# Kernel tuning notes

Hardware: AMD Instinct MI355X
Metric: run time of the kernel (lower is better)

## Reference

```python
import jax, jax.numpy as jnp
import numpy as np

DIM, HEADS, K = 128, 4, 7
HD = DIM // HEADS


def _nbr_idx(n, k):
    # NATTEN boundary-clamped neighborhood (dilation=1): window start clamped to [0, n-k]
    i = np.arange(n)
    start = np.clip(i - k // 2, 0, n - k)
    idx = start[:, None] + np.arange(k)[None, :]          # (n, k) absolute neighbor index
    rel = idx - i[:, None] + (k - 1)                      # (n, k) index into 2k-1 rpb axis
    return jnp.asarray(idx), jnp.asarray(rel)


def _ln(x, w, b, eps=1e-5):
    mu = jnp.mean(x, -1, keepdims=True)
    var = jnp.var(x, -1, keepdims=True)
    return (x - mu) * jax.lax.rsqrt(var + eps) * w + b


def setup_inputs() -> dict:
    key = jax.random.key(0)
    ks = jax.random.split(key, 16)
    B, H, W, C = 1, 128, 128, DIM
    f = jax.random.normal
    inp = {
        'x': f(ks[0], (B, H, W, C), jnp.float32),
        'y': f(ks[1], (B, H, W, C), jnp.float32),
        'qv_w': f(ks[2], (2 * C, C), jnp.float32) * 0.02,
        'qv_b': jnp.zeros((2 * C,), jnp.float32),
        'k_w': f(ks[3], (C, C), jnp.float32) * 0.02,
        'k_b': jnp.zeros((C,), jnp.float32),
        'rpb': f(ks[4], (HEADS, 2 * K - 1, 2 * K - 1), jnp.float32) * 0.02,
        'proj_w': f(ks[5], (C, C), jnp.float32) * 0.02,
        'proj_b': jnp.zeros((C,), jnp.float32),
        'n1_w': jnp.ones((C,), jnp.float32),
        'n1_b': jnp.zeros((C,), jnp.float32),
        'n2_w': jnp.ones((C,), jnp.float32),
        'n2_b': jnp.zeros((C,), jnp.float32),
        'fc1_w': f(ks[6], (4 * C, C), jnp.float32) * 0.02,
        'fc1_b': jnp.zeros((4 * C,), jnp.float32),
        'fc2_w': f(ks[7], (C, 4 * C), jnp.float32) * 0.02,
        'fc2_b': jnp.zeros((C,), jnp.float32),
    }
    return inp


def _block(x, y, qv_w, qv_b, k_w, k_b, rpb, proj_w, proj_b,
           n1_w, n1_b, n2_w, n2_b, fc1_w, fc1_b, fc2_w, fc2_b):
    B, H, W, C = x.shape
    scale = HD ** -0.5
    # ---- CrossNat2D attention on norm1(x) vs y ----
    xn = _ln(x, n1_w, n1_b)
    qv = xn @ qv_w.T + qv_b                               # (B,H,W,2C)
    q = qv[..., :C].reshape(B, H, W, HEADS, HD) * scale
    v = qv[..., C:].reshape(B, H, W, HEADS, HD)
    k = (y @ k_w.T + k_b).reshape(B, H, W, HEADS, HD)

    idx_h, rel_h = _nbr_idx(H, K)
    idx_w, rel_w = _nbr_idx(W, K)
    # gather neighborhoods: (B, H, K, W, K, HEADS, HD)
    k_nbr = k[:, idx_h][:, :, :, idx_w]
    v_nbr = v[:, idx_h][:, :, :, idx_w]

    # attention logits over KxK neighborhood
    attn = jnp.einsum('bijhd,biajchd->bijhac', q, k_nbr)  # (B,H,W,heads,K,K)
    bias = rpb[:, rel_h][..., rel_w]                      # (heads,H,K,W,K)
    attn = attn + jnp.transpose(bias, (1, 3, 0, 2, 4))    # broadcast over B
    attn = jax.nn.softmax(attn.reshape(B, H, W, HEADS, K * K), axis=-1)
    attn = attn.reshape(B, H, W, HEADS, K, K)

    out = jnp.einsum('bijhac,biajchd->bijhd', attn, v_nbr).reshape(B, H, W, C)
    out = out @ proj_w.T + proj_b

    x = x + out
    # ---- MLP ----
    h = _ln(x, n2_w, n2_b) @ fc1_w.T + fc1_b
    h = jax.nn.gelu(h, approximate=False) @ fc2_w.T + fc2_b
    return x + h


def reference(x, y, qv_w, qv_b, k_w, k_b, rpb, proj_w, proj_b,
              n1_w, n1_b, n2_w, n2_b, fc1_w, fc1_b, fc2_w, fc2_b):
    return _block(x, y, qv_w, qv_b, k_w, k_b, rpb, proj_w, proj_b,
                  n1_w, n1_b, n2_w, n2_b, fc1_w, fc1_b, fc2_w, fc2_b)
```

## Files before the change

kernel.cpp:

```cpp
#include <hip/hip_runtime.h>
#include <hip/hip_bf16.h>


#define N_PIX 16384
#define C 128
#define HEADS 4
#define HD 32
#define HW 128

typedef __hip_bfloat16 bf16;
typedef __attribute__((ext_vector_type(8))) short bf16x8;
typedef __attribute__((ext_vector_type(4))) float f32x4;

__device__ __forceinline__ short f2bs(float f) {
    unsigned int r;
    asm("v_cvt_pk_bf16_f32 %0, %1, %2" : "=v"(r) : "v"(f), "v"(f));
    return (short)(r & 0xffff);
}
__device__ __forceinline__ unsigned int pack2(float a, float b) {
    unsigned int r;
    asm("v_cvt_pk_bf16_f32 %0, %1, %2" : "=v"(r) : "v"(a), "v"(b));
    return r;
}
__device__ __forceinline__ float bs2f(short s) {
    __hip_bfloat16_raw r; r.x = (unsigned short)s;
    return __bfloat162float(__hip_bfloat16(r));
}
__device__ __forceinline__ float gelu_f(float v) {
    const float z2 = v * (2.302236206f + 0.102943322f * v * v);
    return v / (1.f + exp2f(-z2));
}

__global__ __launch_bounds__(256) void k_wconv(
    const float* __restrict__ qv_w, const float* __restrict__ k_w,
    const float* __restrict__ proj_w, const float* __restrict__ fc1_w,
    const float* __restrict__ fc2_w,
    short* __restrict__ wqv, short* __restrict__ wk, short* __restrict__ wproj,
    short* __restrict__ wfc1, short* __restrict__ wfc2) {
    const int i = blockIdx.x * 256 + threadIdx.x;
    if (i < 32768) wqv[i] = f2bs(qv_w[i]);
    if (i < 16384) { wk[i] = f2bs(k_w[i]); wproj[i] = f2bs(proj_w[i]); }
    if (i < 65536) { wfc1[i] = f2bs(fc1_w[i]); wfc2[i] = f2bs(fc2_w[i]); }
}

__global__ __launch_bounds__(256, 4) void k_qkv(
    const float* __restrict__ x, const float* __restrict__ y,
    const short* __restrict__ wqv, const float* __restrict__ qv_b,
    const short* __restrict__ wk, const float* __restrict__ k_b,
    const float* __restrict__ n1_w, const float* __restrict__ n1_b,
    bf16* __restrict__ qb, bf16* __restrict__ vb, bf16* __restrict__ kb) {
    __shared__ short xn[16][136];
    __shared__ short yl[16][136];
    const int t = threadIdx.x;
    const int pix0 = (blockIdx.x & 7) * 2048 + (blockIdx.x >> 3) * 16;
    {
        const int r = t >> 4, ch8 = (t & 15) * 8;
        const size_t gp = (size_t)(pix0 + r) * C + ch8;
        float xv[8], yv[8];
        *(float4*)&xv[0] = *(const float4*)(x + gp);
        *(float4*)&xv[4] = *(const float4*)(x + gp + 4);
        *(float4*)&yv[0] = *(const float4*)(y + gp);
        *(float4*)&yv[4] = *(const float4*)(y + gp + 4);
        float sm = 0.f, sq = 0.f;
#pragma unroll
        for (int i2 = 0; i2 < 8; i2++) { sm += xv[i2]; sq += xv[i2] * xv[i2]; }
#pragma unroll
        for (int msk = 1; msk < 16; msk <<= 1) {
            sm += __shfl_xor(sm, msk, 64); sq += __shfl_xor(sq, msk, 64);
        }
        const float mu = sm * (1.f / 128.f);
        const float ri = rsqrtf(sq * (1.f / 128.f) - mu * mu + 1e-5f);
        float w1[8], b1[8];
        *(float4*)&w1[0] = *(const float4*)(n1_w + ch8);
        *(float4*)&w1[4] = *(const float4*)(n1_w + ch8 + 4);
        *(float4*)&b1[0] = *(const float4*)(n1_b + ch8);
        *(float4*)&b1[4] = *(const float4*)(n1_b + ch8 + 4);
        uint4 xp, yp;
        xp.x = pack2((xv[0] - mu) * ri * w1[0] + b1[0], (xv[1] - mu) * ri * w1[1] + b1[1]);
        xp.y = pack2((xv[2] - mu) * ri * w1[2] + b1[2], (xv[3] - mu) * ri * w1[3] + b1[3]);
        xp.z = pack2((xv[4] - mu) * ri * w1[4] + b1[4], (xv[5] - mu) * ri * w1[5] + b1[5]);
        xp.w = pack2((xv[6] - mu) * ri * w1[6] + b1[6], (xv[7] - mu) * ri * w1[7] + b1[7]);
        yp.x = pack2(yv[0], yv[1]); yp.y = pack2(yv[2], yv[3]);
        yp.z = pack2(yv[4], yv[5]); yp.w = pack2(yv[6], yv[7]);
        *(uint4*)&xn[r][ch8] = xp;
        *(uint4*)&yl[r][ch8] = yp;
    }
    __syncthreads();
    const int wave = t >> 6, lane = t & 63, quad = lane >> 4, l15 = lane & 15;
    const float scale = 0.1767766952966369f;
    {
        bf16x8 aA[4];
#pragma unroll
        for (int kt = 0; kt < 4; kt++)
            aA[kt] = *(const bf16x8*)&xn[l15][kt * 32 + quad * 8];
#pragma unroll
        for (int s = 0; s < 4; s++) {
            const int n = (wave + 4 * s) * 16 + l15;
            f32x4 acc = {0.f, 0.f, 0.f, 0.f};
#pragma unroll
            for (int kt = 0; kt < 4; kt++) {
                bf16x8 b = *(const bf16x8*)&wqv[n * C + kt * 32 + quad * 8];
                acc = __builtin_amdgcn_mfma_f32_16x16x32_bf16(aA[kt], b, acc, 0, 0, 0);
            }
            const float bias = qv_b[n];
#pragma unroll
            for (int r = 0; r < 4; r++) {
                const int m = quad * 4 + r;
                const float v = acc[r] + bias;
                if (s < 2) qb[(size_t)(pix0 + m) * C + n] = __float2bfloat16(v * scale);
                else       vb[(size_t)(pix0 + m) * C + (n - C)] = __float2bfloat16(v);
            }
        }
    }
    {
        bf16x8 aY[4];
#pragma unroll
        for (int kt = 0; kt < 4; kt++)
            aY[kt] = *(const bf16x8*)&yl[l15][kt * 32 + quad * 8];
        const int n0 = (wave * 2) * 16 + l15, n1 = (wave * 2 + 1) * 16 + l15;
        f32x4 a0 = {0.f, 0.f, 0.f, 0.f}, a1 = {0.f, 0.f, 0.f, 0.f};
#pragma unroll
        for (int kt = 0; kt < 4; kt++) {
            bf16x8 b0 = *(const bf16x8*)&wk[n0 * C + kt * 32 + quad * 8];
            bf16x8 b1 = *(const bf16x8*)&wk[n1 * C + kt * 32 + quad * 8];
            a0 = __builtin_amdgcn_mfma_f32_16x16x32_bf16(aY[kt], b0, a0, 0, 0, 0);
            a1 = __builtin_amdgcn_mfma_f32_16x16x32_bf16(aY[kt], b1, a1, 0, 0, 0);
        }
        const float b0s = k_b[n0], b1s = k_b[n1];
#pragma unroll
        for (int r = 0; r < 4; r++) {
            const int m = quad * 4 + r;
            kb[(size_t)(pix0 + m) * C + n0] = __float2bfloat16(a0[r] + b0s);
            kb[(size_t)(pix0 + m) * C + n1] = __float2bfloat16(a1[r] + b1s);
        }
    }
}

__global__ __launch_bounds__(512, 4) void k_fam(
    const bf16* __restrict__ qb, const bf16* __restrict__ kb,
    const bf16* __restrict__ vb, const float* __restrict__ rpb,
    const float* __restrict__ x,
    const short* __restrict__ wproj, const float* __restrict__ proj_b,
    const float* __restrict__ n2_w, const float* __restrict__ n2_b,
    const short* __restrict__ wfc1, const float* __restrict__ fc1_b,
    const short* __restrict__ wfc2, const float* __restrict__ fc2_b,
    float* __restrict__ out) {
    __shared__ short KP[19008];
    __shared__ short Vl[19008];
    __shared__ float muA[32], riA[32];
    short* const Pm  = KP;
    short* const aoL = KP;
    short* const x1b = KP + 4352;
    short* const xnb = KP + 8704;
    short* const hb  = Vl;
    const int t = threadIdx.x;
    const int wave = t >> 6, lane = t & 63, quad = lane >> 4, l15 = lane & 15;
    const int h = wave & 3, mt = wave >> 2;
    const int s_ = blockIdx.x >> 3;
    const int i0 = ((blockIdx.x & 7) * 2 + (s_ >> 5)) * 8;
    const int j0 = (s_ & 31) * 4;
    const int rs = min(max(i0 - 3, 0), 114);
    const int cs = min(max(j0 - 3, 0), 118);
    const int mA = mt * 16 + l15;
    const int pA = (i0 + (mA >> 2)) * HW + j0 + (mA & 3);
    const bf16x8 aQ = *(const bf16x8*)(qb + (size_t)pA * C + h * HD + quad * 8);
    const int nR0 = h * 16 + l15, nR1 = (h + 4) * 16 + l15;
    float xres0[4], xres1[4];
#pragma unroll
    for (int r = 0; r < 4; r++) {
        const int m = mt * 16 + quad * 4 + r;
        const int p = (i0 + (m >> 2)) * HW + j0 + (m & 3);
        xres0[r] = x[(size_t)p * C + nR0];
        xres1[r] = x[(size_t)p * C + nR1];
    }
    {
        const int seg = t & 15, r0 = t >> 4;
        const int q0 = (r0 * 13) >> 7;
        const int m0 = r0 - q0 * 10;
#pragma unroll
        for (int half = 0; half < 2; half++) {
            const bf16* __restrict__ src = half ? vb : kb;
            short* const dst = half ? Vl : KP;
            int r = r0, q = q0, rm = m0;
#pragma unroll
            for (int it = 0; it < 5; it++) {
                if (r < 140) {
                    const size_t g = (size_t)((rs + q) * HW + cs + rm) * C + seg * 8;
                    *(uint4*)&dst[r * 132 + seg * 8] = *(const uint4*)(src + g);
                }
                r += 32; q += 3; rm += 2;
                if (rm >= 10) { rm -= 10; q += 1; }
            }
        }
    }
    __syncthreads();
    f32x4 S[9];
#pragma unroll
    for (int nt = 0; nt < 9; nt++) {
        const bf16x8 bK = *(const bf16x8*)&KP[(nt * 16 + l15) * 132 + h * HD + quad * 8];
        f32x4 z = {0.f, 0.f, 0.f, 0.f};
        S[nt] = __builtin_amdgcn_mfma_f32_16x16x32_bf16(aQ, bK, z, 0, 0, 0);
    }
    const float* rpbh = rpb + h * 169;
    int aiA[9], ajA[9];
    {
        int ai = rs + (l15 >= 10 ? 1 : 0);
        int aj = cs + (l15 >= 10 ? l15 - 10 : l15);
        const int cb = cs + 10;
#pragma unroll
        for (int nt = 0; nt < 9; nt++) {
            aiA[nt] = ai; ajA[nt] = aj;
            aj += 6; ai += 1;
            if (aj >= cb) { aj -= 10; ai += 1; }
        }
    }
    float smx[4];
#pragma unroll
    for (int r = 0; r < 4; r++) {
        const int m = mt * 16 + quad * 4 + r;
        const int i = i0 + (m >> 2), j = j0 + (m & 3);
        const int shi = min(max(i - 3, 0), 121);
        const int swj = min(max(j - 3, 0), 121);
        float best = -1e30f;
#pragma unroll
        for (int nt = 0; nt < 9; nt++) {
            const int ai = aiA[nt], aj = ajA[nt];
            const bool vnb = (nt < 8) | (l15 < 12);
            const bool valid = vnb & (ai >= shi) & (ai <= shi + 6) & (aj >= swj) & (aj <= swj + 6);
            const int ri = min(max(ai - i + 6, 0), 12);
            const int rj = min(max(aj - j + 6, 0), 12);
            const float v = valid ? (S[nt][r] + rpbh[ri * 13 + rj]) : -1e30f;
            S[nt][r] = v;
            best = fmaxf(best, v);
        }
        for (int msk = 1; msk < 16; msk <<= 1) best = fmaxf(best, __shfl_xor(best, msk, 64));
        float s = 0.f;
#pragma unroll
        for (int nt = 0; nt < 9; nt++) {
            const float e = __expf(S[nt][r] - best);
            S[nt][r] = e;
            s += e;
        }
        for (int msk = 1; msk < 16; msk <<= 1) s += __shfl_xor(s, msk, 64);
        smx[r] = 1.f / s;
    }
    __syncthreads();
#pragma unroll
    for (int r = 0; r < 4; r++) {
        short* prow = &Pm[(wave * 16 + quad * 4 + r) * 144];
#pragma unroll
        for (int nt = 0; nt < 9; nt++)
            prow[nt * 16 + l15] = f2bs(S[nt][r] * smx[r]);
    }
    f32x4 O0 = {0.f, 0.f, 0.f, 0.f}, O1 = {0.f, 0.f, 0.f, 0.f};
#pragma unroll
    for (int kt = 0; kt < 4; kt++) {
        const bf16x8 aP = *(const bf16x8*)&Pm[(wave * 16 + l15) * 144 + kt * 32 + quad * 8];
#pragma unroll
        for (int nt2 = 0; nt2 < 2; nt2++) {
            const int ch = h * HD + nt2 * 16 + l15;
            const int base = (kt * 32 + quad * 8) * 132 + ch;
            bf16x8 bV;
#pragma unroll
            for (int jj = 0; jj < 8; jj++) bV[jj] = Vl[base + jj * 132];
            if (nt2 == 0) O0 = __builtin_amdgcn_mfma_f32_16x16x32_bf16(aP, bV, O0, 0, 0, 0);
            else          O1 = __builtin_amdgcn_mfma_f32_16x16x32_bf16(aP, bV, O1, 0, 0, 0);
        }
    }
    {
        const bf16x8 aP = *(const bf16x8*)&Pm[(wave * 16 + l15) * 144 + 128 + quad * 8];
#pragma unroll
        for (int nt2 = 0; nt2 < 2; nt2++) {
            const int ch = h * HD + nt2 * 16 + l15;
            bf16x8 bV = {0, 0, 0, 0, 0, 0, 0, 0};
            if (quad == 0) {
                const int base = 128 * 132 + ch;
#pragma unroll
                for (int jj = 0; jj < 8; jj++) bV[jj] = Vl[base + jj * 132];
            } else if (quad == 1) {
                const int base = 136 * 132 + ch;
#pragma unroll
                for (int jj = 0; jj < 4; jj++) bV[jj] = Vl[base + jj * 132];
            }
            if (nt2 == 0) O0 = __builtin_amdgcn_mfma_f32_16x16x32_bf16(aP, bV, O0, 0, 0, 0);
            else          O1 = __builtin_amdgcn_mfma_f32_16x16x32_bf16(aP, bV, O1, 0, 0, 0);
        }
    }
    bf16x8 wp0[4], wp1[4];
#pragma unroll
    for (int kt = 0; kt < 4; kt++) {
        wp0[kt] = *(const bf16x8*)&wproj[nR0 * C + kt * 32 + quad * 8];
        wp1[kt] = *(const bf16x8*)&wproj[nR1 * C + kt * 32 + quad * 8];
    }
    __syncthreads();
#pragma unroll
    for (int r = 0; r < 4; r++) {
        const int m = mt * 16 + quad * 4 + r;
        aoL[m * 136 + h * HD + l15] = f2bs(O0[r]);
        aoL[m * 136 + h * HD + 16 + l15] = f2bs(O1[r]);
    }
    __syncthreads();
    float x1f0[4], x1f1[4];
    {
        bf16x8 aO[4];
#pragma unroll
        for (int kt = 0; kt < 4; kt++)
            aO[kt] = *(const bf16x8*)&aoL[(mt * 16 + l15) * 136 + kt * 32 + quad * 8];
        f32x4 a0 = {0.f, 0.f, 0.f, 0.f}, a1 = {0.f, 0.f, 0.f, 0.f};
#pragma unroll
        for (int kt = 0; kt < 4; kt++) {
            a0 = __builtin_amdgcn_mfma_f32_16x16x32_bf16(aO[kt], wp0[kt], a0, 0, 0, 0);
            a1 = __builtin_amdgcn_mfma_f32_16x16x32_bf16(aO[kt], wp1[kt], a1, 0, 0, 0);
        }
        const float b0s = proj_b[nR0], b1s = proj_b[nR1];
#pragma unroll
        for (int r = 0; r < 4; r++) {
            const int m = mt * 16 + quad * 4 + r;
            const float v0 = xres0[r] + a0[r] + b0s;
            const float v1 = xres1[r] + a1[r] + b1s;
            x1f0[r] = v0; x1f1[r] = v1;
            x1b[m * 136 + nR0] = f2bs(v0);
            x1b[m * 136 + nR1] = f2bs(v1);
        }
    }
    __syncthreads();
    {
        const int r = t >> 4, c8 = (t & 15) * 8;
        const short* p = &x1b[r * 136 + c8];
        float sm = 0.f, sq = 0.f;
#pragma unroll
        for (int i2 = 0; i2 < 8; i2++) {
            const float v = bs2f(p[i2]); sm += v; sq += v * v;
        }
#pragma unroll
        for (int msk = 1; msk < 16; msk <<= 1) {
            sm += __shfl_xor(sm, msk, 64); sq += __shfl_xor(sq, msk, 64);
        }
        if ((t & 15) == 0) {
            const float mu = sm * (1.f / 128.f);
            const float var = sq * (1.f / 128.f) - mu * mu;
            muA[r] = mu; riA[r] = rsqrtf(var + 1e-5f);
        }
    }
    __syncthreads();
    for (int e = t; e < 32 * 128; e += 512) {
        const int r = e >> 7, c = e & 127;
        xnb[r * 136 + c] = f2bs((bs2f(x1b[r * 136 + c]) - muA[r]) * riA[r] * n2_w[c] + n2_b[c]);
    }
    __syncthreads();
    {
        bf16x8 aX[4];
#pragma unroll
        for (int kt = 0; kt < 4; kt++)
            aX[kt] = *(const bf16x8*)&xnb[(mt * 16 + l15) * 136 + kt * 32 + quad * 8];
#pragma unroll
        for (int a = 0; a < 4; a++) {
            const int n0 = (h + 8 * a) * 16 + l15, n1 = (h + 8 * a + 4) * 16 + l15;
            f32x4 a0 = {0.f, 0.f, 0.f, 0.f}, a1 = {0.f, 0.f, 0.f, 0.f};
#pragma unroll
            for (int kt = 0; kt < 4; kt++) {
                bf16x8 b0 = *(const bf16x8*)&wfc1[n0 * C + kt * 32 + quad * 8];
                bf16x8 b1 = *(const bf16x8*)&wfc1[n1 * C + kt * 32 + quad * 8];
                a0 = __builtin_amdgcn_mfma_f32_16x16x32_bf16(aX[kt], b0, a0, 0, 0, 0);
                a1 = __builtin_amdgcn_mfma_f32_16x16x32_bf16(aX[kt], b1, a1, 0, 0, 0);
            }
            const float b0s = fc1_b[n0], b1s = fc1_b[n1];
#pragma unroll
            for (int r = 0; r < 4; r++) {
                const int m = mt * 16 + quad * 4 + r;
                hb[m * 520 + n0] = f2bs(gelu_f(a0[r] + b0s));
                hb[m * 520 + n1] = f2bs(gelu_f(a1[r] + b1s));
            }
        }
    }
    __syncthreads();
    {
        f32x4 a0 = {0.f, 0.f, 0.f, 0.f}, a1 = {0.f, 0.f, 0.f, 0.f};
#pragma unroll
        for (int kt = 0; kt < 16; kt++) {
            const bf16x8 aP = *(const bf16x8*)&hb[(mt * 16 + l15) * 520 + kt * 32 + quad * 8];
            bf16x8 b0 = *(const bf16x8*)&wfc2[nR0 * 512 + kt * 32 + quad * 8];
            bf16x8 b1 = *(const bf16x8*)&wfc2[nR1 * 512 + kt * 32 + quad * 8];
            a0 = __builtin_amdgcn_mfma_f32_16x16x32_bf16(aP, b0, a0, 0, 0, 0);
            a1 = __builtin_amdgcn_mfma_f32_16x16x32_bf16(aP, b1, a1, 0, 0, 0);
        }
        const float b0s = fc2_b[nR0], b1s = fc2_b[nR1];
#pragma unroll
        for (int r = 0; r < 4; r++) {
            const int m = mt * 16 + quad * 4 + r;
            const int p = (i0 + (m >> 2)) * HW + j0 + (m & 3);
            out[(size_t)p * C + nR0] = a0[r] + b0s + x1f0[r];
            out[(size_t)p * C + nR1] = a1[r] + b1s + x1f1[r];
        }
    }
}

extern "C" void kernel_launch(void* const* d_in, const int* in_sizes, int n_in,
                              void* d_out, int out_size, void* d_ws, size_t ws_size,
                              hipStream_t stream) {
    const float* x      = (const float*)d_in[0];
    const float* y      = (const float*)d_in[1];
    const float* qv_w   = (const float*)d_in[2];
    const float* qv_b   = (const float*)d_in[3];
    const float* k_w    = (const float*)d_in[4];
    const float* k_b    = (const float*)d_in[5];
    const float* rpb    = (const float*)d_in[6];
    const float* proj_w = (const float*)d_in[7];
    const float* proj_b = (const float*)d_in[8];
    const float* n1_w   = (const float*)d_in[9];
    const float* n1_b   = (const float*)d_in[10];
    const float* n2_w   = (const float*)d_in[11];
    const float* n2_b   = (const float*)d_in[12];
    const float* fc1_w  = (const float*)d_in[13];
    const float* fc1_b  = (const float*)d_in[14];
    const float* fc2_w  = (const float*)d_in[15];
    const float* fc2_b  = (const float*)d_in[16];
    float* out = (float*)d_out;

    bf16* qb  = (bf16*)d_ws;
    bf16* vb  = qb + (size_t)N_PIX * C;
    bf16* kb  = vb + (size_t)N_PIX * C;
    short* wqv  = (short*)(kb + (size_t)N_PIX * C);
    short* wk   = wqv + 32768;
    short* wproj= wk + 16384;
    short* wfc1 = wproj + 16384;
    short* wfc2 = wfc1 + 65536;

    k_wconv<<<256, 256, 0, stream>>>(qv_w, k_w, proj_w, fc1_w, fc2_w,
                                     wqv, wk, wproj, wfc1, wfc2);
    k_qkv<<<1024, 256, 0, stream>>>(x, y, wqv, qv_b, wk, k_b, n1_w, n1_b,
                                    qb, vb, kb);
    k_fam<<<512, 512, 0, stream>>>(qb, kb, vb, rpb, x, wproj, proj_b, n2_w, n2_b,
                                   wfc1, fc1_b, wfc2, fc2_b, out);
}
```

Before: 160.4 us.

## Enlarge fused attention+MLP tile to 8x8 pixels with shared 14x14 K/V halo

```diff
diff --git a/kernel.cpp b/kernel.cpp
--- a/kernel.cpp
+++ b/kernel.cpp
@@ -136,7 +136,7 @@
     }
 }
 
-__global__ __launch_bounds__(512, 4) void k_fam(
+__global__ __launch_bounds__(512, 2) void k_fam(
     const bf16* __restrict__ qb, const bf16* __restrict__ kb,
     const bf16* __restrict__ vb, const float* __restrict__ rpb,
     const float* __restrict__ x,
@@ -145,252 +145,318 @@
     const short* __restrict__ wfc1, const float* __restrict__ fc1_b,
     const short* __restrict__ wfc2, const float* __restrict__ fc2_b,
     float* __restrict__ out) {
-    __shared__ short KP[19008];
-    __shared__ short Vl[19008];
-    __shared__ float muA[32], riA[32];
-    short* const Pm  = KP;
-    short* const aoL = KP;
-    short* const x1b = KP + 4352;
-    short* const xnb = KP + 8704;
-    short* const hb  = Vl;
+    __shared__ short SH[67104];
+    short* const KU  = SH;
+    short* const VU  = SH + 25872;
+    short* const Pb  = SH + 51744;
+    short* const aoL = SH;
+    short* const xnb = SH + 8448;
+    short* const hb  = SH + 16896;
+    short* const x1b = SH + 51744;
     const int t = threadIdx.x;
     const int wave = t >> 6, lane = t & 63, quad = lane >> 4, l15 = lane & 15;
     const int h = wave & 3, mt = wave >> 2;
-    const int s_ = blockIdx.x >> 3;
-    const int i0 = ((blockIdx.x & 7) * 2 + (s_ >> 5)) * 8;
-    const int j0 = (s_ & 31) * 4;
+    const int p = wave & 1, g = wave >> 1;
+    const int tile = (blockIdx.x & 7) * 32 + (blockIdx.x >> 3);
+    const int i0 = (tile >> 4) * 8, j0 = (tile & 15) * 8;
     const int rs = min(max(i0 - 3, 0), 114);
-    const int cs = min(max(j0 - 3, 0), 118);
-    const int mA = mt * 16 + l15;
-    const int pA = (i0 + (mA >> 2)) * HW + j0 + (mA & 3);
-    const bf16x8 aQ = *(const bf16x8*)(qb + (size_t)pA * C + h * HD + quad * 8);
-    const int nR0 = h * 16 + l15, nR1 = (h + 4) * 16 + l15;
-    float xres0[4], xres1[4];
-#pragma unroll
-    for (int r = 0; r < 4; r++) {
-        const int m = mt * 16 + quad * 4 + r;
-        const int p = (i0 + (m >> 2)) * HW + j0 + (m & 3);
-        xres0[r] = x[(size_t)p * C + nR0];
-        xres1[r] = x[(size_t)p * C + nR1];
+    const int cs2 = min(max(j0 - 3, 0), 114);
+    const int n_0 = (2 * g) * 16 + l15, n_1 = (2 * g + 1) * 16 + l15;
+    bf16x8 aQv[2];
+#pragma unroll
+    for (int u = 0; u < 2; u++) {
+        const int q = mt * 2 + u;
+        const int iq = i0 + (q >> 1) * 4, jq = j0 + (q & 1) * 4;
+        const int pA = (iq + (l15 >> 2)) * HW + jq + (l15 & 3);
+        aQv[u] = *(const bf16x8*)(qb + (size_t)pA * C + h * HD + quad * 8);
+    }
+    float xres[2][2][4];
+#pragma unroll
+    for (int u = 0; u < 2; u++) {
+        const int qm = 2 * p + u;
+        const int ib = i0 + (qm >> 1) * 4 + quad, jb = j0 + (qm & 1) * 4;
+#pragma unroll
+        for (int r = 0; r < 4; r++) {
+            const size_t pp = (size_t)(ib * HW + jb + r) * C;
+            xres[u][0][r] = x[pp + n_0];
+            xres[u][1][r] = x[pp + n_1];
+        }
     }
     {
         const int seg = t & 15, r0 = t >> 4;
-        const int q0 = (r0 * 13) >> 7;
-        const int m0 = r0 - q0 * 10;
-#pragma unroll
-        for (int half = 0; half < 2; half++) {
-            const bf16* __restrict__ src = half ? vb : kb;
-            short* const dst = half ? Vl : KP;
-            int r = r0, q = q0, rm = m0;
-#pragma unroll
-            for (int it = 0; it < 5; it++) {
-                if (r < 140) {
-                    const size_t g = (size_t)((rs + q) * HW + cs + rm) * C + seg * 8;
-                    *(uint4*)&dst[r * 132 + seg * 8] = *(const uint4*)(src + g);
+        int q14 = (r0 >= 28) ? 2 : (r0 >= 14 ? 1 : 0);
+        int m14 = r0 - 14 * q14;
+        int r = r0;
+#pragma unroll
+        for (int it = 0; it < 7; it++) {
+            if (r < 196) {
+                const size_t gp = (size_t)((rs + q14) * HW + (cs2 + m14)) * C + seg * 8;
+                *(uint4*)&KU[r * 132 + seg * 8] = *(const uint4*)(kb + gp);
+                *(uint4*)&VU[r * 132 + seg * 8] = *(const uint4*)(vb + gp);
+            }
+            r += 32; q14 += 2; m14 += 4;
+            if (m14 >= 14) { m14 -= 14; q14 += 1; }
+        }
+    }
+    int nrA[7], ncA[7];
+    {
+        int nr = (l15 >= 10) ? 1 : 0;
+        int nc = l15 - ((l15 >= 10) ? 10 : 0);
+#pragma unroll
+        for (int nt = 0; nt < 7; nt++) {
+            nrA[nt] = nr; ncA[nt] = nc;
+            nc += 6; nr += 1;
+            if (nc >= 10) { nc -= 10; nr += 1; }
+        }
+    }
+    __syncthreads();
+    const float* rpbh = rpb + h * 169;
+    f32x4 Oacc[2][2];
+#pragma unroll
+    for (int u = 0; u < 2; u++) {
+        Oacc[u][0] = (f32x4){0.f, 0.f, 0.f, 0.f};
+        Oacc[u][1] = (f32x4){0.f, 0.f, 0.f, 0.f};
+    }
+#pragma unroll
+    for (int u = 0; u < 2; u++) {
+        const int q = mt * 2 + u;
+        const int iq = i0 + (q >> 1) * 4, jq = j0 + (q & 1) * 4;
+        const int rq = min(max(iq - 3, 0), 118), cq = min(max(jq - 3, 0), 118);
+        const int vbase = (rq - rs) * 14 + (cq - cs2);
+        f32x4 S[7];
+#pragma unroll
+        for (int nt = 0; nt < 7; nt++) {
+            const int lr = min(vbase + nrA[nt] * 14 + ncA[nt], 195);
+            const bf16x8 bK = *(const bf16x8*)&KU[lr * 132 + h * HD + quad * 8];
+            f32x4 z = {0.f, 0.f, 0.f, 0.f};
+            S[nt] = __builtin_amdgcn_mfma_f32_16x16x32_bf16(aQv[u], bK, z, 0, 0, 0);
+        }
+        float smx[4];
+#pragma unroll
+        for (int r = 0; r < 4; r++) {
+            const int i = iq + quad, j = jq + r;
+            const int shi = min(max(i - 3, 0), 121);
+            const int swj = min(max(j - 3, 0), 121);
+            float best = -1e30f;
+#pragma unroll
+            for (int nt = 0; nt < 7; nt++) {
+                const int ai = rq + nrA[nt], aj = cq + ncA[nt];
+                const bool vnb = (nt < 6) | (l15 < 4);
+                const bool valid = vnb & (ai >= shi) & (ai <= shi + 6) & (aj >= swj) & (aj <= swj + 6);
+                const int ri = min(max(ai - i + 6, 0), 12);
+                const int rj = min(max(aj - j + 6, 0), 12);
+                const float v = valid ? (S[nt][r] + rpbh[ri * 13 + rj]) : -1e30f;
+                S[nt][r] = v;
+                best = fmaxf(best, v);
+            }
+            for (int msk = 1; msk < 16; msk <<= 1) best = fmaxf(best, __shfl_xor(best, msk, 64));
+            float s = 0.f;
+#pragma unroll
+            for (int nt = 0; nt < 7; nt++) {
+                const float e = __expf(S[nt][r] - best);
+                S[nt][r] = e;
+                s += e;
+            }
+            for (int msk = 1; msk < 16; msk <<= 1) s += __shfl_xor(s, msk, 64);
+            smx[r] = 1.f / s;
+        }
+#pragma unroll
+        for (int r = 0; r < 4; r++) {
+            short* prow = &Pb[(wave * 16 + quad * 4 + r) * 120];
+#pragma unroll
+            for (int nt = 0; nt < 7; nt++)
+                prow[nt * 16 + l15] = f2bs(S[nt][r] * smx[r]);
+        }
+#pragma unroll
+        for (int kt = 0; kt < 3; kt++) {
+            const bf16x8 aP = *(const bf16x8*)&Pb[(wave * 16 + l15) * 120 + kt * 32 + quad * 8];
+            const int kbase = kt * 32 + quad * 8;
+            int kr = (kbase * 205) >> 11;
+            int kc = kbase - 10 * kr;
+            int sidx = vbase + kr * 14 + kc;
+            int lvr[8];
+#pragma unroll
+            for (int jj = 0; jj < 8; jj++) {
+                lvr[jj] = sidx;
+                kc++; sidx++;
+                if (kc >= 10) { kc = 0; sidx += 4; }
+            }
+#pragma unroll
+            for (int nt2 = 0; nt2 < 2; nt2++) {
+                const int ch = h * HD + nt2 * 16 + l15;
+                bf16x8 bV;
+#pragma unroll
+                for (int jj = 0; jj < 8; jj++) bV[jj] = VU[lvr[jj] * 132 + ch];
+                Oacc[u][nt2] = __builtin_amdgcn_mfma_f32_16x16x32_bf16(aP, bV, Oacc[u][nt2], 0, 0, 0);
+            }
+        }
+        {
+            bf16x8 aP = {0, 0, 0, 0, 0, 0, 0, 0};
+            if (quad < 2) aP = *(const bf16x8*)&Pb[(wave * 16 + l15) * 120 + 96 + quad * 8];
+#pragma unroll
+            for (int nt2 = 0; nt2 < 2; nt2++) {
+                const int ch = h * HD + nt2 * 16 + l15;
+                bf16x8 bV = {0, 0, 0, 0, 0, 0, 0, 0};
+                if (quad == 0) {
+#pragma unroll
+                    for (int jj = 0; jj < 8; jj++) {
+                        const int kc3 = (6 + jj > 9) ? 9 : 6 + jj;
+                        bV[jj] = VU[(vbase + 126 + kc3) * 132 + ch];
+                    }
                 }
-                r += 32; q += 3; rm += 2;
-                if (rm >= 10) { rm -= 10; q += 1; }
-            }
-        }
-    }
-    __syncthreads();
-    f32x4 S[9];
-#pragma unroll
-    for (int nt = 0; nt < 9; nt++) {
-        const bf16x8 bK = *(const bf16x8*)&KP[(nt * 16 + l15) * 132 + h * HD + quad * 8];
-        f32x4 z = {0.f, 0.f, 0.f, 0.f};
-        S[nt] = __builtin_amdgcn_mfma_f32_16x16x32_bf16(aQ, bK, z, 0, 0, 0);
-    }
-    const float* rpbh = rpb + h * 169;
-    int aiA[9], ajA[9];
-    {
-        int ai = rs + (l15 >= 10 ? 1 : 0);
-        int aj = cs + (l15 >= 10 ? l15 - 10 : l15);
-        const int cb = cs + 10;
-#pragma unroll
-        for (int nt = 0; nt < 9; nt++) {
-            aiA[nt] = ai; ajA[nt] = aj;
-            aj += 6; ai += 1;
-            if (aj >= cb) { aj -= 10; ai += 1; }
-        }
-    }
-    float smx[4];
-#pragma unroll
-    for (int r = 0; r < 4; r++) {
-        const int m = mt * 16 + quad * 4 + r;
-        const int i = i0 + (m >> 2), j = j0 + (m & 3);
-        const int shi = min(max(i - 3, 0), 121);
-        const int swj = min(max(j - 3, 0), 121);
-        float best = -1e30f;
-#pragma unroll
-        for (int nt = 0; nt < 9; nt++) {
-            const int ai = aiA[nt], aj = ajA[nt];
-            const bool vnb = (nt < 8) | (l15 < 12);
-            const bool valid = vnb & (ai >= shi) & (ai <= shi + 6) & (aj >= swj) & (aj <= swj + 6);
-            const int ri = min(max(ai - i + 6, 0), 12);
-            const int rj = min(max(aj - j + 6, 0), 12);
-            const float v = valid ? (S[nt][r] + rpbh[ri * 13 + rj]) : -1e30f;
-            S[nt][r] = v;
-            best = fmaxf(best, v);
-        }
-        for (int msk = 1; msk < 16; msk <<= 1) best = fmaxf(best, __shfl_xor(best, msk, 64));
-        float s = 0.f;
-#pragma unroll
-        for (int nt = 0; nt < 9; nt++) {
-            const float e = __expf(S[nt][r] - best);
-            S[nt][r] = e;
-            s += e;
-        }
-        for (int msk = 1; msk < 16; msk <<= 1) s += __shfl_xor(s, msk, 64);
-        smx[r] = 1.f / s;
-    }
-    __syncthreads();
-#pragma unroll
-    for (int r = 0; r < 4; r++) {
-        short* prow = &Pm[(wave * 16 + quad * 4 + r) * 144];
-#pragma unroll
-        for (int nt = 0; nt < 9; nt++)
-            prow[nt * 16 + l15] = f2bs(S[nt][r] * smx[r]);
-    }
-    f32x4 O0 = {0.f, 0.f, 0.f, 0.f}, O1 = {0.f, 0.f, 0.f, 0.f};
+                Oacc[u][nt2] = __builtin_amdgcn_mfma_f32_16x16x32_bf16(aP, bV, Oacc[u][nt2], 0, 0, 0);
+            }
+        }
+    }
+    bf16x8 wp0[4], wp1[4];
 #pragma unroll
     for (int kt = 0; kt < 4; kt++) {
-        const bf16x8 aP = *(const bf16x8*)&Pm[(wave * 16 + l15) * 144 + kt * 32 + quad * 8];
-#pragma unroll
-        for (int nt2 = 0; nt2 < 2; nt2++) {
-            const int ch = h * HD + nt2 * 16 + l15;
-            const int base = (kt * 32 + quad * 8) * 132 + ch;
-            bf16x8 bV;
-#pragma unroll
-            for (int jj = 0; jj < 8; jj++) bV[jj] = Vl[base + jj * 132];
-            if (nt2 == 0) O0 = __builtin_amdgcn_mfma_f32_16x16x32_bf16(aP, bV, O0, 0, 0, 0);
-            else          O1 = __builtin_amdgcn_mfma_f32_16x16x32_bf16(aP, bV, O1, 0, 0, 0);
-        }
-    }
-    {
-        const bf16x8 aP = *(const bf16x8*)&Pm[(wave * 16 + l15) * 144 + 128 + quad * 8];
-#pragma unroll
-        for (int nt2 = 0; nt2 < 2; nt2++) {
-            const int ch = h * HD + nt2 * 16 + l15;
-            bf16x8 bV = {0, 0, 0, 0, 0, 0, 0, 0};
-            if (quad == 0) {
-                const int base = 128 * 132 + ch;
-#pragma unroll
-                for (int jj = 0; jj < 8; jj++) bV[jj] = Vl[base + jj * 132];
-            } else if (quad == 1) {
-                const int base = 136 * 132 + ch;
-#pragma unroll
-                for (int jj = 0; jj < 4; jj++) bV[jj] = Vl[base + jj * 132];
-            }
-            if (nt2 == 0) O0 = __builtin_amdgcn_mfma_f32_16x16x32_bf16(aP, bV, O0, 0, 0, 0);
-            else          O1 = __builtin_amdgcn_mfma_f32_16x16x32_bf16(aP, bV, O1, 0, 0, 0);
-        }
-    }
-    bf16x8 wp0[4], wp1[4];
-#pragma unroll
-    for (int kt = 0; kt < 4; kt++) {
-        wp0[kt] = *(const bf16x8*)&wproj[nR0 * C + kt * 32 + quad * 8];
-        wp1[kt] = *(const bf16x8*)&wproj[nR1 * C + kt * 32 + quad * 8];
-    }
-    __syncthreads();
-#pragma unroll
-    for (int r = 0; r < 4; r++) {
-        const int m = mt * 16 + quad * 4 + r;
-        aoL[m * 136 + h * HD + l15] = f2bs(O0[r]);
-        aoL[m * 136 + h * HD + 16 + l15] = f2bs(O1[r]);
-    }
-    __syncthreads();
-    float x1f0[4], x1f1[4];
-    {
-        bf16x8 aO[4];
-#pragma unroll
-        for (int kt = 0; kt < 4; kt++)
-            aO[kt] = *(const bf16x8*)&aoL[(mt * 16 + l15) * 136 + kt * 32 + quad * 8];
-        f32x4 a0 = {0.f, 0.f, 0.f, 0.f}, a1 = {0.f, 0.f, 0.f, 0.f};
+        wp0[kt] = *(const bf16x8*)&wproj[n_0 * C + kt * 32 + quad * 8];
+        wp1[kt] = *(const bf16x8*)&wproj[n_1 * C + kt * 32 + quad * 8];
+    }
+    __syncthreads();
+#pragma unroll
+    for (int u = 0; u < 2; u++) {
+        const int q = mt * 2 + u;
+#pragma unroll
+        for (int r = 0; r < 4; r++) {
+            const int m = q * 16 + quad * 4 + r;
+            aoL[m * 132 + h * HD + l15] = f2bs(Oacc[u][0][r]);
+            aoL[m * 132 + h * HD + 16 + l15] = f2bs(Oacc[u][1][r]);
+        }
+    }
+    __syncthreads();
+    float x1f[2][2][4];
+    {
+        bf16x8 aO[2][4];
+#pragma unroll
+        for (int u = 0; u < 2; u++)
+#pragma unroll
+            for (int kt = 0; kt < 4; kt++)
+                aO[u][kt] = *(const bf16x8*)&aoL[((2 * p + u) * 16 + l15) * 132 + kt * 32 + quad * 8];
+        f32x4 pa[2][2];
+        pa[0][0] = (f32x4){0.f, 0.f, 0.f, 0.f}; pa[0][1] = (f32x4){0.f, 0.f, 0.f, 0.f};
+        pa[1][0] = (f32x4){0.f, 0.f, 0.f, 0.f}; pa[1][1] = (f32x4){0.f, 0.f, 0.f, 0.f};
 #pragma unroll
         for (int kt = 0; kt < 4; kt++) {
-            a0 = __builtin_amdgcn_mfma_f32_16x16x32_bf16(aO[kt], wp0[kt], a0, 0, 0, 0);
-            a1 = __builtin_amdgcn_mfma_f32_16x16x32_bf16(aO[kt], wp1[kt], a1, 0, 0, 0);
-        }
-        const float b0s = proj_b[nR0], b1s = proj_b[nR1];
-#pragma unroll
-        for (int r = 0; r < 4; r++) {
-            const int m = mt * 16 + quad * 4 + r;
-            const float v0 = xres0[r] + a0[r] + b0s;
-            const float v1 = xres1[r] + a1[r] + b1s;
-            x1f0[r] = v0; x1f1[r] = v1;
-            x1b[m * 136 + nR0] = f2bs(v0);
-            x1b[m * 136 + nR1] = f2bs(v1);
-        }
-    }
-    __syncthreads();
-    {
-        const int r = t >> 4, c8 = (t & 15) * 8;
-        const short* p = &x1b[r * 136 + c8];
+            pa[0][0] = __builtin_amdgcn_mfma_f32_16x16x32_bf16(aO[0][kt], wp0[kt], pa[0][0], 0, 0, 0);
+            pa[0][1] = __builtin_amdgcn_mfma_f32_16x16x32_bf16(aO[0][kt], wp1[kt], pa[0][1], 0, 0, 0);
+            pa[1][0] = __builtin_amdgcn_mfma_f32_16x16x32_bf16(aO[1][kt], wp0[kt], pa[1][0], 0, 0, 0);
+            pa[1][1] = __builtin_amdgcn_mfma_f32_16x16x32_bf16(aO[1][kt], wp1[kt], pa[1][1], 0, 0, 0);
+        }
+        const float b0s = proj_b[n_0], b1s = proj_b[n_1];
+#pragma unroll
+        for (int u = 0; u < 2; u++) {
+#pragma unroll
+            for (int r = 0; r < 4; r++) {
+                const int m = (2 * p + u) * 16 + quad * 4 + r;
+                const float v0 = xres[u][0][r] + pa[u][0][r] + b0s;
+                const float v1 = xres[u][1][r] + pa[u][1][r] + b1s;
+                x1f[u][0][r] = v0; x1f[u][1][r] = v1;
+                x1b[m * 132 + n_0] = f2bs(v0);
+                x1b[m * 132 + n_1] = f2bs(v1);
+            }
+        }
+    }
+    __syncthreads();
+    {
+        const int row = t >> 3, c16 = (t & 7) * 16;
+        float xv[16];
+        {
+            const uint4 d0 = *(const uint4*)&x1b[row * 132 + c16];
+            const uint4 d1 = *(const uint4*)&x1b[row * 132 + c16 + 8];
+            const unsigned int w[8] = {d0.x, d0.y, d0.z, d0.w, d1.x, d1.y, d1.z, d1.w};
+#pragma unroll
+            for (int i2 = 0; i2 < 8; i2++) {
+                xv[2 * i2]     = bs2f((short)(w[i2] & 0xffff));
+                xv[2 * i2 + 1] = bs2f((short)(w[i2] >> 16));
+            }
+        }
         float sm = 0.f, sq = 0.f;
 #pragma unroll
-        for (int i2 = 0; i2 < 8; i2++) {
-            const float v = bs2f(p[i2]); sm += v; sq += v * v;
-        }
-#pragma unroll
-        for (int msk = 1; msk < 16; msk <<= 1) {
+        for (int i2 = 0; i2 < 16; i2++) { sm += xv[i2]; sq += xv[i2] * xv[i2]; }
+#pragma unroll
+        for (int msk = 1; msk < 8; msk <<= 1) {
             sm += __shfl_xor(sm, msk, 64); sq += __shfl_xor(sq, msk, 64);
         }
-        if ((t & 15) == 0) {
-            const float mu = sm * (1.f / 128.f);
-            const float var = sq * (1.f / 128.f) - mu * mu;
-            muA[r] = mu; riA[r] = rsqrtf(var + 1e-5f);
-        }
-    }
-    __syncthreads();
-    for (int e = t; e < 32 * 128; e += 512) {
-        const int r = e >> 7, c = e & 127;
-        xnb[r * 136 + c] = f2bs((bs2f(x1b[r * 136 + c]) - muA[r]) * riA[r] * n2_w[c] + n2_b[c]);
-    }
-    __syncthreads();
-    {
-        bf16x8 aX[4];
-#pragma unroll
-        for (int kt = 0; kt < 4; kt++)
-            aX[kt] = *(const bf16x8*)&xnb[(mt * 16 + l15) * 136 + kt * 32 + quad * 8];
-#pragma unroll
-        for (int a = 0; a < 4; a++) {
-            const int n0 = (h + 8 * a) * 16 + l15, n1 = (h + 8 * a + 4) * 16 + l15;
-            f32x4 a0 = {0.f, 0.f, 0.f, 0.f}, a1 = {0.f, 0.f, 0.f, 0.f};
+        const float mu = sm * (1.f / 128.f);
+        const float ri = rsqrtf(sq * (1.f / 128.f) - mu * mu + 1e-5f);
+        float w2[16], b2[16];
+        *(float4*)&w2[0]  = *(const float4*)(n2_w + c16);
+        *(float4*)&w2[4]  = *(const float4*)(n2_w + c16 + 4);
+        *(float4*)&w2[8]  = *(const float4*)(n2_w + c16 + 8);
+        *(float4*)&w2[12] = *(const float4*)(n2_w + c16 + 12);
+        *(float4*)&b2[0]  = *(const float4*)(n2_b + c16);
+        *(float4*)&b2[4]  = *(const float4*)(n2_b + c16 + 4);
+        *(float4*)&b2[8]  = *(const float4*)(n2_b + c16 + 8);
+        *(float4*)&b2[12] = *(const float4*)(n2_b + c16 + 12);
+        uint4 o0, o1;
+        o0.x = pack2((xv[0] - mu) * ri * w2[0] + b2[0],   (xv[1] - mu) * ri * w2[1] + b2[1]);
+        o0.y = pack2((xv[2] - mu) * ri * w2[2] + b2[2],   (xv[3] - mu) * ri * w2[3] + b2[3]);
+        o0.z = pack2((xv[4] - mu) * ri * w2[4] + b2[4],   (xv[5] - mu) * ri * w2[5] + b2[5]);
+        o0.w = pack2((xv[6] - mu) * ri * w2[6] + b2[6],   (xv[7] - mu) * ri * w2[7] + b2[7]);
+        o1.x = pack2((xv[8] - mu) * ri * w2[8] + b2[8],   (xv[9] - mu) * ri * w2[9] + b2[9]);
+        o1.y = pack2((xv[10] - mu) * ri * w2[10] + b2[10], (xv[11] - mu) * ri * w2[11] + b2[11]);
+        o1.z = pack2((xv[12] - mu) * ri * w2[12] + b2[12], (xv[13] - mu) * ri * w2[13] + b2[13]);
+        o1.w = pack2((xv[14] - mu) * ri * w2[14] + b2[14], (xv[15] - mu) * ri * w2[15] + b2[15]);
+        *(uint4*)&xnb[row * 132 + c16] = o0;
+        *(uint4*)&xnb[row * 132 + c16 + 8] = o1;
+    }
+    __syncthreads();
+    {
+        bf16x8 aX[2][4];
+#pragma unroll
+        for (int u = 0; u < 2; u++)
+#pragma unroll
+            for (int kt = 0; kt < 4; kt++)
+                aX[u][kt] = *(const bf16x8*)&xnb[((2 * p + u) * 16 + l15) * 132 + kt * 32 + quad * 8];
+#pragma unroll
+        for (int a = 0; a < 8; a++) {
+            const int n = (g * 8 + a) * 16 + l15;
+            f32x4 c0 = {0.f, 0.f, 0.f, 0.f}, c1 = {0.f, 0.f, 0.f, 0.f};
 #pragma unroll
             for (int kt = 0; kt < 4; kt++) {
-                bf16x8 b0 = *(const bf16x8*)&wfc1[n0 * C + kt * 32 + quad * 8];
-                bf16x8 b1 = *(const bf16x8*)&wfc1[n1 * C + kt * 32 + quad * 8];
-                a0 = __builtin_amdgcn_mfma_f32_16x16x32_bf16(aX[kt], b0, a0, 0, 0, 0);
-                a1 = __builtin_amdgcn_mfma_f32_16x16x32_bf16(aX[kt], b1, a1, 0, 0, 0);
-            }
-            const float b0s = fc1_b[n0], b1s = fc1_b[n1];
+                const bf16x8 bw = *(const bf16x8*)&wfc1[n * C + kt * 32 + quad * 8];
+                c0 = __builtin_amdgcn_mfma_f32_16x16x32_bf16(aX[0][kt], bw, c0, 0, 0, 0);
+                c1 = __builtin_amdgcn_mfma_f32_16x16x32_bf16(aX[1][kt], bw, c1, 0, 0, 0);
+            }
+            const float bias = fc1_b[n];
 #pragma unroll
             for (int r = 0; r < 4; r++) {
-                const int m = mt * 16 + quad * 4 + r;
-                hb[m * 520 + n0] = f2bs(gelu_f(a0[r] + b0s));
-                hb[m * 520 + n1] = f2bs(gelu_f(a1[r] + b1s));
-            }
-        }
-    }
-    __syncthreads();
-    {
-        f32x4 a0 = {0.f, 0.f, 0.f, 0.f}, a1 = {0.f, 0.f, 0.f, 0.f};
+                const int m0 = (2 * p) * 16 + quad * 4 + r;
+                hb[m0 * 520 + n] = f2bs(gelu_f(c0[r] + bias));
+                hb[(m0 + 16) * 520 + n] = f2bs(gelu_f(c1[r] + bias));
+            }
+        }
+    }
+    __syncthreads();
+    {
+        f32x4 f00 = {0.f, 0.f, 0.f, 0.f}, f01 = {0.f, 0.f, 0.f, 0.f};
+        f32x4 f10 = {0.f, 0.f, 0.f, 0.f}, f11 = {0.f, 0.f, 0.f, 0.f};
 #pragma unroll
         for (int kt = 0; kt < 16; kt++) {
-            const bf16x8 aP = *(const bf16x8*)&hb[(mt * 16 + l15) * 520 + kt * 32 + quad * 8];
-            bf16x8 b0 = *(const bf16x8*)&wfc2[nR0 * 512 + kt * 32 + quad * 8];
-            bf16x8 b1 = *(const bf16x8*)&wfc2[nR1 * 512 + kt * 32 + quad * 8];
-            a0 = __builtin_amdgcn_mfma_f32_16x16x32_bf16(aP, b0, a0, 0, 0, 0);
-            a1 = __builtin_amdgcn_mfma_f32_16x16x32_bf16(aP, b1, a1, 0, 0, 0);
-        }
-        const float b0s = fc2_b[nR0], b1s = fc2_b[nR1];
-#pragma unroll
-        for (int r = 0; r < 4; r++) {
-            const int m = mt * 16 + quad * 4 + r;
-            const int p = (i0 + (m >> 2)) * HW + j0 + (m & 3);
-            out[(size_t)p * C + nR0] = a0[r] + b0s + x1f0[r];
-            out[(size_t)p * C + nR1] = a1[r] + b1s + x1f1[r];
+            const bf16x8 a0 = *(const bf16x8*)&hb[((2 * p) * 16 + l15) * 520 + kt * 32 + quad * 8];
+            const bf16x8 a1 = *(const bf16x8*)&hb[((2 * p + 1) * 16 + l15) * 520 + kt * 32 + quad * 8];
+            const bf16x8 w0 = *(const bf16x8*)&wfc2[n_0 * 512 + kt * 32 + quad * 8];
+            const bf16x8 w1 = *(const bf16x8*)&wfc2[n_1 * 512 + kt * 32 + quad * 8];
+            f00 = __builtin_amdgcn_mfma_f32_16x16x32_bf16(a0, w0, f00, 0, 0, 0);
+            f01 = __builtin_amdgcn_mfma_f32_16x16x32_bf16(a0, w1, f01, 0, 0, 0);
+            f10 = __builtin_amdgcn_mfma_f32_16x16x32_bf16(a1, w0, f10, 0, 0, 0);
+            f11 = __builtin_amdgcn_mfma_f32_16x16x32_bf16(a1, w1, f11, 0, 0, 0);
+        }
+        const float b0s = fc2_b[n_0], b1s = fc2_b[n_1];
+#pragma unroll
+        for (int u = 0; u < 2; u++) {
+            const int qm = 2 * p + u;
+            const int ib = i0 + (qm >> 1) * 4 + quad, jb = j0 + (qm & 1) * 4;
+#pragma unroll
+            for (int r = 0; r < 4; r++) {
+                const size_t pp = (size_t)(ib * HW + jb + r) * C;
+                const float v0 = (u ? f10[r] : f00[r]) + b0s + x1f[u][0][r];
+                const float v1 = (u ? f11[r] : f01[r]) + b1s + x1f[u][1][r];
+                out[pp + n_0] = v0;
+                out[pp + n_1] = v1;
+            }
         }
     }
 }
@@ -430,6 +496,6 @@
                                      wqv, wk, wproj, wfc1, wfc2);
     k_qkv<<<1024, 256, 0, stream>>>(x, y, wqv, qv_b, wk, k_b, n1_w, n1_b,
                                     qb, vb, kb);
-    k_fam<<<512, 512, 0, stream>>>(qb, kb, vb, rpb, x, wproj, proj_b, n2_w, n2_b,
+    k_fam<<<256, 512, 0, stream>>>(qb, kb, vb, rpb, x, wproj, proj_b, n2_w, n2_b,
                                    wfc1, fc1_b, wfc2, fc2_b, out);
 }
```

After: 152.6 us. 4.9% less time.
